# Optimization experiments

Hardware: AMD Instinct MI355X
Metric: run time of the kernel (lower is better)

The kernel has to match this reference:

```python
import jax, jax.numpy as jnp
import numpy as np

B, FEW, NN = 4096, 5, 64
D = 128            # embed_dim
NSYM = 100000
DM = 2 * D         # d_model = 256
DI = 2 * DM        # support-encoder inner = 512
H = 2 * DM         # LSTMCell hidden = 512
STEPS = 4          # process_steps


def setup_inputs() -> dict:
    key = jax.random.key(0)
    cnt = [0]
    def nk():
        cnt[0] += 1
        return jax.random.fold_in(key, cnt[0])
    def nrm(shape, scale=0.05):
        return jax.random.normal(nk(), shape, dtype=jnp.float32) * scale
    def ridx(shape):
        return jax.random.randint(nk(), shape, 0, NSYM, dtype=jnp.int32)
    inp = {}
    inp['q_l1'] = ridx((B, NN, 2)); inp['q_l2'] = ridx((B, NN, 2))
    inp['q_r1'] = ridx((B, NN, 2)); inp['q_r2'] = ridx((B, NN, 2))
    inp['s_l1'] = ridx((FEW, NN, 2)); inp['s_l2'] = ridx((FEW, NN, 2))
    inp['s_r1'] = ridx((FEW, NN, 2)); inp['s_r2'] = ridx((FEW, NN, 2))
    inp['q_deg_l'] = jax.random.randint(nk(), (B,), 1, NN, dtype=jnp.int32)
    inp['q_deg_r'] = jax.random.randint(nk(), (B,), 1, NN, dtype=jnp.int32)
    inp['s_deg_l'] = jax.random.randint(nk(), (FEW,), 1, NN, dtype=jnp.int32)
    inp['s_deg_r'] = jax.random.randint(nk(), (FEW,), 1, NN, dtype=jnp.int32)
    inp['emb'] = nrm((NSYM + 1, D)).at[NSYM].set(0.0)  # padding_idx row = 0
    inp['gcn_w'] = nrm((D, 2 * D))
    inp['gcn_wb'] = nrm((D,))
    inp['gcn_b'] = jnp.zeros((D,), jnp.float32)
    inp['hop_gate'] = jnp.ones((2,), jnp.float32)
    inp['attn_w'] = nrm((1, D))
    inp['attn_b'] = jnp.zeros((1,), jnp.float32)
    inp['p1_w'] = nrm((DI, DM)); inp['p1_b'] = jnp.zeros((DI,), jnp.float32)
    inp['p2_w'] = nrm((DM, DI)); inp['p2_b'] = jnp.zeros((DM,), jnp.float32)
    inp['ln_g'] = jnp.ones((DM,), jnp.float32); inp['ln_b'] = jnp.zeros((DM,), jnp.float32)
    inp['w_ih'] = nrm((4 * H, DM)); inp['w_hh'] = nrm((4 * H, H))
    inp['b_ih'] = jnp.zeros((4 * H,), jnp.float32); inp['b_hh'] = jnp.zeros((4 * H,), jnp.float32)
    return inp


def _neighbor_encoder(conn, emb, gcn_w, gcn_wb, gcn_b, attn_w, attn_b):
    # conn: [N, NN, 2] (relation id, entity id)
    e = emb[conn]                                     # [N, NN, 2, D]
    concat = e.reshape(conn.shape[0], conn.shape[1], 2 * D)  # cat(rel, ent)
    proj = concat @ gcn_w.T + gcn_wb + gcn_b          # [N, NN, D]
    scores = (proj @ attn_w.T + attn_b)[..., 0]       # [N, NN]
    w = jax.nn.softmax(scores, axis=1)[..., None]
    return jnp.tanh(jnp.sum(proj * w, axis=1))        # [N, D]


def _support_encoder(x, p1_w, p1_b, p2_w, p2_b, ln_g, ln_b):
    out = jax.nn.relu(x @ p1_w.T + p1_b) @ p2_w.T + p2_b
    z = out + x
    mu = jnp.mean(z, axis=-1, keepdims=True)
    var = jnp.var(z, axis=-1, keepdims=True)
    return (z - mu) / jnp.sqrt(var + 1e-6) * ln_g + ln_b


def _query_encoder(support_g, q, w_ih, w_hh, b_ih, b_hh):
    # matching-networks 'process' LSTM attention, STEPS fixed iterations
    h_r = jnp.zeros((q.shape[0], H), q.dtype)
    c = jnp.zeros_like(h_r)
    h = q
    for _ in range(STEPS):
        gates = q @ w_ih.T + b_ih + h_r @ w_hh.T + b_hh
        i, f, g, o = jnp.split(gates, 4, axis=-1)
        c = jax.nn.sigmoid(f) * c + jax.nn.sigmoid(i) * jnp.tanh(g)
        h_cell = jax.nn.sigmoid(o) * jnp.tanh(c)
        h = q + h_cell[:, :DM]
        attn = jax.nn.softmax(h @ support_g.T, axis=1)
        r = attn @ support_g
        h_r = jnp.concatenate([h, r], axis=1)
    return h


def reference(q_l1, q_l2, q_r1, q_r2, s_l1, s_l2, s_r1, s_r2,
              q_deg_l, q_deg_r, s_deg_l, s_deg_r,
              emb, gcn_w, gcn_wb, gcn_b, hop_gate, attn_w, attn_b,
              p1_w, p1_b, p2_w, p2_b, ln_g, ln_b, w_ih, w_hh, b_ih, b_hh):
    ne = lambda conn: _neighbor_encoder(conn, emb, gcn_w, gcn_wb, gcn_b, attn_w, attn_b)
    gw = jax.nn.softmax(hop_gate)
    q_left = gw[0] * ne(q_l1) + gw[1] * ne(q_l2)
    q_right = gw[0] * ne(q_r1) + gw[1] * ne(q_r2)
    s_left = gw[0] * ne(s_l1) + gw[1] * ne(s_l2)
    s_right = gw[0] * ne(s_r1) + gw[1] * ne(s_r2)
    query_neighbor = jnp.concatenate([q_left, q_right], axis=-1)    # [B, DM]
    support_neighbor = jnp.concatenate([s_left, s_right], axis=-1)  # [FEW, DM]
    support_g = _support_encoder(support_neighbor, p1_w, p1_b, p2_w, p2_b, ln_g, ln_b)
    query_g = _query_encoder(support_g, query_neighbor, w_ih, w_hh, b_ih, b_hh)
    support_m = jnp.mean(support_g, axis=0, keepdims=True)          # [1, DM]
    return (query_g @ support_m.T)[:, 0]                            # [B]
```

## Files before the change

kernel.cpp:

```cpp
#include <hip/hip_runtime.h>

typedef unsigned short bf16u;
typedef unsigned char u8;
typedef unsigned int u32;
typedef float f32x4 __attribute__((ext_vector_type(4)));
typedef short bf16x8 __attribute__((ext_vector_type(8)));

__device__ inline float sigmoidf_(float x) { return 1.f / (1.f + __expf(-x)); }
__device__ inline float tanhf_(float x) {
  float e = __expf(2.f * x);
  return 1.f - 2.f / (e + 1.f);
}
__device__ inline float b2f(bf16u u) { return __uint_as_float(((u32)u) << 16); }
__device__ inline bf16u f2b(float f) {
  u32 i = __float_as_uint(f);
  u32 r = (i + 0x7fffu + ((i >> 16) & 1u)) >> 16;
  return (bf16u)r;
}
__device__ inline u8 enc8(float v) {
  float q = fmaf(v, 512.f, 128.5f);
  q = fminf(fmaxf(q, 0.f), 255.f);
  return (u8)(int)q;
}
__device__ inline float ub0(u32 u) { return (float)(u & 0xffu); }
__device__ inline float ub1(u32 u) { return (float)((u >> 8) & 0xffu); }
__device__ inline float ub2(u32 u) { return (float)((u >> 16) & 0xffu); }
__device__ inline float ub3(u32 u) { return (float)(u >> 24); }

#define GLOAD16(gsrc, ldst)                                                   \
  __builtin_amdgcn_global_load_lds(                                           \
      (const __attribute__((address_space(1))) void*)(gsrc),                  \
      (__attribute__((address_space(3))) void*)(ldst), 16, 0, 0)

__global__ __launch_bounds__(256) void k_front(
    const float* __restrict__ emb, const float* __restrict__ gcn_w,
    const float* __restrict__ attn_w,
    const float* __restrict__ w_ih, const float* __restrict__ w_hh,
    const float* __restrict__ b_ih, const float* __restrict__ b_hh,
    u8* __restrict__ pr, u8* __restrict__ pe,
    float* __restrict__ srel, float* __restrict__ sent,
    bf16u* __restrict__ WWa, bf16u* __restrict__ WWb, float* __restrict__ bsum,
    bf16u* __restrict__ XX)
{
  const int blk = blockIdx.x, t = threadIdx.x;
  if (blk >= 1563) {
    const int b = blk - 1563;
    if (t < 59) {
      XX[(size_t)b * 576 + 517 + t] = 0;
      XX[(size_t)(b + 2048) * 576 + 517 + t] = 0;
    }
    float wi = w_ih[b * 256 + t];
    float wh = w_hh[b * 512 + t];
    WWa[(size_t)b * 576 + t] = f2b(wi);
    WWb[(size_t)b * 576 + t] = f2b(wi + wh);
    WWb[(size_t)b * 576 + 256 + t] = f2b(wh);
    if (t < 59) WWb[(size_t)b * 576 + 517 + t] = 0;
    if (t == 0) bsum[b] = b_ih[b] + b_hh[b];
    return;
  }
  const int row0 = blk << 6;
  __shared__ short As[64][136];
  __shared__ union PB {
    short B[128][136];
    u8 ob[64][272];
  } pb;
  __shared__ float us[256];
  #pragma unroll
  for (int s = 0; s < 8; ++s) {
    int f = s * 256 + t;
    int row = f >> 4, e0 = (f & 15) * 8;
    float4 v0 = *(const float4*)&gcn_w[row * 256 + e0];
    float4 v1 = *(const float4*)&gcn_w[row * 256 + e0 + 4];
    ushort4 p0, p1;
    p0.x = f2b(v0.x); p0.y = f2b(v0.y); p0.z = f2b(v0.z); p0.w = f2b(v0.w);
    p1.x = f2b(v1.x); p1.y = f2b(v1.y); p1.z = f2b(v1.z); p1.w = f2b(v1.w);
    *(ushort4*)&pb.B[row][e0] = p0;
    *(ushort4*)&pb.B[row][e0 + 4] = p1;
  }
  #pragma unroll
  for (int s = 0; s < 8; ++s) {
    int f = s * 256 + t;
    int row = f >> 5, q = f & 31;
    int gr = row0 + row; if (gr > 100000) gr = 100000;
    float4 v = *(const float4*)&emb[(size_t)gr * 128 + (q << 2)];
    ushort4 pk;
    pk.x = f2b(v.x); pk.y = f2b(v.y); pk.z = f2b(v.z); pk.w = f2b(v.w);
    *(ushort4*)&As[row][q << 2] = pk;
  }
  __syncthreads();
  if (t < 128) {
    float a = 0.f;
    #pragma unroll 8
    for (int d = 0; d < 128; ++d)
      a = fmaf(__uint_as_float(((u32)(unsigned short)pb.B[d][t]) << 16),
               attn_w[d], a);
    us[t] = a;
  }
  const int wave = t >> 6, lane = t & 63;
  const int quad = lane >> 4, l16 = lane & 15;
  const int wm = (wave >> 1) << 5, wn = (wave & 1) << 6;
  f32x4 acc0[2][4], acc1[2][4];
  #pragma unroll
  for (int i = 0; i < 2; ++i)
    #pragma unroll
    for (int j = 0; j < 4; ++j) {
      acc0[i][j] = (f32x4){0.f, 0.f, 0.f, 0.f};
      acc1[i][j] = (f32x4){0.f, 0.f, 0.f, 0.f};
    }
  #pragma unroll
  for (int kc = 0; kc < 4; ++kc) {
    bf16x8 af[2], bfr[4];
    #pragma unroll
    for (int i = 0; i < 2; ++i)
      af[i] = *(const bf16x8*)&As[wm + i * 16 + l16][kc * 32 + quad * 8];
    #pragma unroll
    for (int j = 0; j < 4; ++j)
      bfr[j] = *(const bf16x8*)&pb.B[wn + j * 16 + l16][kc * 32 + quad * 8];
    #pragma unroll
    for (int i = 0; i < 2; ++i)
      #pragma unroll
      for (int j = 0; j < 4; ++j)
        acc0[i][j] = __builtin_amdgcn_mfma_f32_16x16x32_bf16(af[i], bfr[j], acc0[i][j], 0, 0, 0);
  }
  __syncthreads();
  #pragma unroll
  for (int s = 0; s < 8; ++s) {
    int f = s * 256 + t;
    int row = f >> 4, e0 = (f & 15) * 8;
    float4 v0 = *(const float4*)&gcn_w[row * 256 + 128 + e0];
    float4 v1 = *(const float4*)&gcn_w[row * 256 + 128 + e0 + 4];
    ushort4 p0, p1;
    p0.x = f2b(v0.x); p0.y = f2b(v0.y); p0.z = f2b(v0.z); p0.w = f2b(v0.w);
    p1.x = f2b(v1.x); p1.y = f2b(v1.y); p1.z = f2b(v1.z); p1.w = f2b(v1.w);
    *(ushort4*)&pb.B[row][e0] = p0;
    *(ushort4*)&pb.B[row][e0 + 4] = p1;
  }
  __syncthreads();
  if (t < 128) {
    float a = 0.f;
    #pragma unroll 8
    for (int d = 0; d < 128; ++d)
      a = fmaf(__uint_as_float(((u32)(unsigned short)pb.B[d][t]) << 16),
               attn_w[d], a);
    us[128 + t] = a;
  }
  #pragma unroll
  for (int kc = 0; kc < 4; ++kc) {
    bf16x8 af[2], bfr[4];
    #pragma unroll
    for (int i = 0; i < 2; ++i)
      af[i] = *(const bf16x8*)&As[wm + i * 16 + l16][kc * 32 + quad * 8];
    #pragma unroll
    for (int j = 0; j < 4; ++j)
      bfr[j] = *(const bf16x8*)&pb.B[wn + j * 16 + l16][kc * 32 + quad * 8];
    #pragma unroll
    for (int i = 0; i < 2; ++i)
      #pragma unroll
      for (int j = 0; j < 4; ++j)
        acc1[i][j] = __builtin_amdgcn_mfma_f32_16x16x32_bf16(af[i], bfr[j], acc1[i][j], 0, 0, 0);
  }
  __syncthreads();
  {
    const int row = t >> 2, l = t & 3;
    int gr = row0 + row; if (gr > 100000) gr = 100000;
    const short* ar = &As[row][l * 32];
    const float* u0 = &us[l * 32];
    const float* u1 = &us[128 + l * 32];
    float p0 = 0.f, p1 = 0.f;
    #pragma unroll
    for (int i = 0; i < 32; ++i) {
      float e = __uint_as_float(((u32)(unsigned short)ar[i]) << 16);
      p0 += e * u0[i];
      p1 += e * u1[i];
    }
    p0 += __shfl_xor(p0, 1, 64); p0 += __shfl_xor(p0, 2, 64);
    p1 += __shfl_xor(p1, 1, 64); p1 += __shfl_xor(p1, 2, 64);
    if (l == 0) { srel[gr] = p0; sent[gr] = p1; }
  }
  #pragma unroll
  for (int j = 0; j < 4; ++j) {
    const int col = wn + j * 16 + l16;
    #pragma unroll
    for (int i = 0; i < 2; ++i) {
      #pragma unroll
      for (int r = 0; r < 4; ++r) {
        int row = wm + i * 16 + quad * 4 + r;
        pb.ob[row][col] = enc8(acc0[i][j][r]);
        pb.ob[row][128 + col] = enc8(acc1[i][j][r]);
      }
    }
  }
  __syncthreads();
  #pragma unroll
  for (int s = 0; s < 4; ++s) {
    int c = s * 256 + t;
    int row = c >> 4, part = c & 15;
    int gr = row0 + row;
    if (gr <= 100000) {
      uint4 v = *(const uint4*)&pb.ob[row][part * 16];
      if (part < 8) *(uint4*)&pr[(size_t)gr * 128 + part * 16] = v;
      else          *(uint4*)&pe[(size_t)gr * 128 + (part - 8) * 16] = v;
    }
  }
}

__global__ __launch_bounds__(256) void k_neighbor(
    const int* __restrict__ q_l1, const int* __restrict__ q_l2,
    const int* __restrict__ q_r1, const int* __restrict__ q_r2,
    const int* __restrict__ s_l1, const int* __restrict__ s_l2,
    const int* __restrict__ s_r1, const int* __restrict__ s_r2,
    const u8* __restrict__ pr, const u8* __restrict__ pe,
    const float* __restrict__ srel, const float* __restrict__ sent,
    const float* __restrict__ gcn_wb, const float* __restrict__ gcn_b,
    const float* __restrict__ hop_gate,
    float* __restrict__ qn, float* __restrict__ sn, bf16u* __restrict__ XX)
{
  const int b = blockIdx.x, t = threadIdx.x;
  const int *cA, *cB; float* outp; bf16u* xxp; int n, coloff;
  if (b < 4096)      { cA = q_l1; cB = q_l2; n = b;        outp = qn; xxp = XX; coloff = 0; }
  else if (b < 8192) { cA = q_r1; cB = q_r2; n = b - 4096; outp = qn; xxp = XX; coloff = 128; }
  else if (b < 8197) { cA = s_l1; cB = s_l2; n = b - 8192; outp = sn; xxp = 0;  coloff = 0; }
  else               { cA = s_r1; cB = s_r2; n = b - 8197; outp = sn; xxp = 0;  coloff = 128; }

  __shared__ float wS[2][64];
  __shared__ float red[256][17];

  const int hop = t >> 7, g = (t >> 3) & 15, p = t & 7;
  const int* connG = hop ? cB : cA;

  int2 pairs[4];
  #pragma unroll
  for (int kk = 0; kk < 4; ++kk)
    pairs[kk] = *(const int2*)&connG[(n * 64 + g + (kk << 4)) * 2];

  float vR = 0.f, vE = 0.f;
  if (t < 128) {
    const int sh = t >> 6, nn = t & 63;
    const int* connS = sh ? cB : cA;
    int2 sp = *(const int2*)&connS[(n * 64 + nn) * 2];
    vR = srel[sp.x];
    vE = sent[sp.y];
  }

  uint4 ra[4], rb[4];
  #pragma unroll
  for (int kk = 0; kk < 4; ++kk) {
    ra[kk] = *(const uint4*)&pr[(size_t)pairs[kk].x * 128 + p * 16];
    rb[kk] = *(const uint4*)&pe[(size_t)pairs[kk].y * 128 + p * 16];
  }

  if (t < 128) {
    const int sh = t >> 6, nn = t & 63;
    float sc = vR + vE;
    float m = sc;
    #pragma unroll
    for (int off = 32; off; off >>= 1) m = fmaxf(m, __shfl_xor(m, off, 64));
    float e = __expf(sc - m);
    float s = e;
    #pragma unroll
    for (int off = 32; off; off >>= 1) s += __shfl_xor(s, off, 64);
    wS[sh][nn] = e / s;
  }
  __syncthreads();

  float a[16];
  #pragma unroll
  for (int c = 0; c < 16; ++c) a[c] = 0.f;
  #pragma unroll
  for (int kk = 0; kk < 4; ++kk) {
    const float wk = wS[hop][g + (kk << 4)];
    const uint4 A = ra[kk], Bv = rb[kk];
    a[0]  += wk * (ub0(A.x) + ub0(Bv.x));
    a[1]  += wk * (ub1(A.x) + ub1(Bv.x));
    a[2]  += wk * (ub2(A.x) + ub2(Bv.x));
    a[3]  += wk * (ub3(A.x) + ub3(Bv.x));
    a[4]  += wk * (ub0(A.y) + ub0(Bv.y));
    a[5]  += wk * (ub1(A.y) + ub1(Bv.y));
    a[6]  += wk * (ub2(A.y) + ub2(Bv.y));
    a[7]  += wk * (ub3(A.y) + ub3(Bv.y));
    a[8]  += wk * (ub0(A.z) + ub0(Bv.z));
    a[9]  += wk * (ub1(A.z) + ub1(Bv.z));
    a[10] += wk * (ub2(A.z) + ub2(Bv.z));
    a[11] += wk * (ub3(A.z) + ub3(Bv.z));
    a[12] += wk * (ub0(A.w) + ub0(Bv.w));
    a[13] += wk * (ub1(A.w) + ub1(Bv.w));
    a[14] += wk * (ub2(A.w) + ub2(Bv.w));
    a[15] += wk * (ub3(A.w) + ub3(Bv.w));
  }
  #pragma unroll
  for (int c = 0; c < 16; ++c) red[t][c] = a[c];
  __syncthreads();

  if (t < 128) {
    const int d = t, pp = d >> 4, cc = d & 15;
    float sA = 0.f, sB = 0.f;
    #pragma unroll
    for (int gg = 0; gg < 16; ++gg) {
      sA += red[gg * 8 + pp][cc];
      sB += red[128 + gg * 8 + pp][cc];
    }
    float accA = sA * (1.f / 512.f) - 0.5f;
    float accB = sB * (1.f / 512.f) - 0.5f;
    float bias = gcn_wb[d] + gcn_b[d];
    float g0 = hop_gate[0], g1 = hop_gate[1];
    float mx = fmaxf(g0, g1);
    float e0 = __expf(g0 - mx), e1 = __expf(g1 - mx);
    float inv = 1.f / (e0 + e1);
    float v = e0 * inv * tanhf_(bias + accA) + e1 * inv * tanhf_(bias + accB);
    outp[n * 256 + coloff + d] = v;
    if (xxp) xxp[(size_t)n * 576 + coloff + d] = f2b(v);
  }
}

__global__ __launch_bounds__(256) void k_sup1(
    const float* __restrict__ sn, const float* __restrict__ p1_w,
    const float* __restrict__ p1_b, float* __restrict__ h1)
{
  const int r = blockIdx.x >> 3, j0 = (blockIdx.x & 7) << 6;
  const int t = threadIdx.x;
  __shared__ float xs[256];
  xs[t] = sn[r * 256 + t];
  __syncthreads();
  const int j = j0 + (t >> 2), q = t & 3;
  const float* wr = p1_w + (size_t)j * 256 + q * 64;
  float acc = 0.f;
  #pragma unroll
  for (int k = 0; k < 64; ++k) acc += xs[q * 64 + k] * wr[k];
  acc += __shfl_xor(acc, 1, 64);
  acc += __shfl_xor(acc, 2, 64);
  if (q == 0) h1[r * 512 + j] = fmaxf(acc + p1_b[j], 0.f);
}

__global__ __launch_bounds__(256) void k_sup2(
    const float* __restrict__ sn, const float* __restrict__ h1,
    const float* __restrict__ p2_w, const float* __restrict__ p2_b,
    const float* __restrict__ ln_g, const float* __restrict__ ln_b,
    float* __restrict__ sg)
{
  const int r = blockIdx.x, t = threadIdx.x;
  const int lane = t & 63, wave = t >> 6;
  __shared__ float hs[512];
  __shared__ float zs[256];
  __shared__ float r1[4], r2[4];
  hs[t] = h1[r * 512 + t];
  hs[t + 256] = h1[r * 512 + 256 + t];
  __syncthreads();
  const int q = t & 3;
  #pragma unroll
  for (int jc = 0; jc < 4; ++jc) {
    int j = jc * 64 + (t >> 2);
    const float* wr = p2_w + (size_t)j * 512 + q * 128;
    float acc = 0.f;
    #pragma unroll
    for (int k = 0; k < 128; ++k) acc += hs[q * 128 + k] * wr[k];
    acc += __shfl_xor(acc, 1, 64);
    acc += __shfl_xor(acc, 2, 64);
    if (q == 0) zs[j] = acc + p2_b[j] + sn[r * 256 + j];
  }
  __syncthreads();
  float v = zs[t];
  float s1 = v, s2 = v * v;
  #pragma unroll
  for (int off = 32; off; off >>= 1) { s1 += __shfl_xor(s1, off, 64); s2 += __shfl_xor(s2, off, 64); }
  if (lane == 0) { r1[wave] = s1; r2[wave] = s2; }
  __syncthreads();
  float S1 = r1[0] + r1[1] + r1[2] + r1[3];
  float S2 = r2[0] + r2[1] + r2[2] + r2[3];
  float mu = S1 * (1.f / 256.f);
  float var = S2 * (1.f / 256.f) - mu * mu;
  sg[r * 256 + t] = (v - mu) * rsqrtf(var + 1e-6f) * ln_g[t] + ln_b[t];
}

__global__ __launch_bounds__(256) void k_gates_mfma(
    const bf16u* __restrict__ XX, const bf16u* __restrict__ WW,
    const float* __restrict__ bsum, bf16u* __restrict__ gates, int kchunks,
    const float* __restrict__ sg, const float* __restrict__ w_hh,
    bf16u* __restrict__ WWbo, float* __restrict__ sm, int dosg2)
{
  const int t = threadIdx.x;
  const int wave = t >> 6, lane = t & 63;
  const int quad = lane >> 4, l16 = lane & 15;
  const int wm = (wave >> 1) << 6, wn = (wave & 1) << 6;
  const int lin = (blockIdx.x & 7) * 56 + (blockIdx.x >> 3);
  const int row0 = (lin / 14) << 7;
  const int col0 = (lin % 14) << 7;
  __shared__ short As[2][128][64];
  __shared__ short Bs[2][128][64];

  if (dosg2 && blockIdx.x < 32) {
    float (*s5)[256] = (float(*)[256])&As[0][0][0];
    const int blk = blockIdx.x;
    for (int i = t; i < 1280; i += 256) s5[i >> 8][i & 255] = sg[i];
    __syncthreads();
    if (blk == 0)
      sm[t] = (s5[0][t] + s5[1][t] + s5[2][t] + s5[3][t] + s5[4][t]) * 0.2f;
    const int j = (blk << 6) + (t >> 2), q = t & 3;
    const float4* wr = (const float4*)(w_hh + (size_t)j * 512 + 256 + q * 64);
    float a[5] = {0.f, 0.f, 0.f, 0.f, 0.f};
    #pragma unroll
    for (int kk = 0; kk < 16; ++kk) {
      float4 w = wr[kk];
      int k = q * 64 + kk * 4;
      #pragma unroll
      for (int r = 0; r < 5; ++r)
        a[r] += s5[r][k] * w.x + s5[r][k+1] * w.y + s5[r][k+2] * w.z + s5[r][k+3] * w.w;
    }
    #pragma unroll
    for (int r = 0; r < 5; ++r) {
      a[r] += __shfl_xor(a[r], 1, 64);
      a[r] += __shfl_xor(a[r], 2, 64);
    }
    if (q == 0) {
      #pragma unroll
      for (int r = 0; r < 5; ++r)
        WWbo[(size_t)j * 576 + 512 + r] = f2b(a[r]);
    }
    __syncthreads();
  }

  f32x4 acc[4][4];
  #pragma unroll
  for (int i = 0; i < 4; ++i)
    #pragma unroll
    for (int j = 0; j < 4; ++j) acc[i][j] = (f32x4){0.f, 0.f, 0.f, 0.f};

  int offX[4], offW[4];
  #pragma unroll
  for (int e = 0; e < 4; ++e) {
    int row = wave * 32 + e * 8 + (lane >> 3);
    int sw = (lane & 7) ^ (lane >> 3);
    offX[e] = (row0 + row) * 576 + sw * 8;
    offW[e] = (col0 + row) * 576 + sw * 8;
  }
  char* aBase = (char*)&As[0][0][0] + wave * 4096;
  char* bBase = (char*)&Bs[0][0][0] + wave * 4096;

  #define STAGE(buf, kc)                                                      \
    {                                                                         \
      const int kof_ = (kc) * 64;                                             \
      _Pragma("unroll")                                                       \
      for (int e = 0; e < 4; ++e) {                                           \
        GLOAD16(XX + offX[e] + kof_, aBase + (buf) * 16384 + e * 1024);       \
        GLOAD16(WW + offW[e] + kof_, bBase + (buf) * 16384 + e * 1024);       \
      }                                                                       \
    }

  STAGE(0, 0);
  __syncthreads();

  for (int kc = 0; kc < kchunks; ++kc) {
    const int cur = kc & 1;
    if (kc + 1 < kchunks) STAGE(cur ^ 1, kc + 1);
    #pragma unroll
    for (int kc2 = 0; kc2 < 2; ++kc2) {
      bf16x8 af[4], bfr[4];
      #pragma unroll
      for (int i = 0; i < 4; ++i)
        af[i] = *(const bf16x8*)&As[cur][wm + i * 16 + l16]
                                       [(((kc2 << 2) + quad) ^ (l16 & 7)) << 3];
      #pragma unroll
      for (int j = 0; j < 4; ++j)
        bfr[j] = *(const bf16x8*)&Bs[cur][wn + j * 16 + l16]
                                        [(((kc2 << 2) + quad) ^ (l16 & 7)) << 3];
      #pragma unroll
      for (int i = 0; i < 4; ++i)
        #pragma unroll
        for (int j = 0; j < 4; ++j)
          acc[i][j] = __builtin_amdgcn_mfma_f32_16x16x32_bf16(af[i], bfr[j], acc[i][j], 0, 0, 0);
    }
    __syncthreads();
  }
  #undef STAGE

  #pragma unroll
  for (int j = 0; j < 4; ++j) {
    const int col = col0 + wn + j * 16 + l16;
    const float bs = bsum[col];
    #pragma unroll
    for (int i = 0; i < 4; ++i) {
      #pragma unroll
      for (int r = 0; r < 4; ++r) {
        int row = row0 + wm + i * 16 + quad * 4 + r;
        gates[(size_t)row * 2048 + col] = f2b(acc[i][j][r] + bs);
      }
    }
  }
}

__global__ __launch_bounds__(256) void k_cell(
    const bf16u* __restrict__ gates, const float* __restrict__ qn,
    float* __restrict__ c, bf16u* __restrict__ XX,
    const float* __restrict__ sg, const float* __restrict__ sm,
    float* __restrict__ out, int step)
{
  __shared__ float red[4][6];
  const int b = blockIdx.x, t = threadIdx.x;
  const int lane = t & 63, wave = t >> 6;
  const bf16u* g = gates + (size_t)b * 2048;
  float i0 = b2f(g[t]),       f0 = b2f(g[512 + t]), gg0 = b2f(g[1024 + t]), o0 = b2f(g[1536 + t]);
  float i1 = b2f(g[256 + t]), f1 = b2f(g[768 + t]), gg1 = b2f(g[1280 + t]);
  float co0 = step ? c[b * 512 + t] : 0.f;
  float co1 = step ? c[b * 512 + 256 + t] : 0.f;
  float c0 = sigmoidf_(f0) * co0 + sigmoidf_(i0) * tanhf_(gg0);
  float c1 = sigmoidf_(f1) * co1 + sigmoidf_(i1) * tanhf_(gg1);
  if (step < 3) {
    c[b * 512 + t] = c0;
    c[b * 512 + 256 + t] = c1;
  }
  float hcv = sigmoidf_(o0) * tanhf_(c0);
  float h = qn[b * 256 + t] + hcv;
  if (step < 3) {
    XX[(size_t)b * 576 + 256 + t] = f2b(hcv);
    float dots[5];
    #pragma unroll
    for (int s = 0; s < 5; ++s) dots[s] = h * sg[s * 256 + t];
    #pragma unroll
    for (int off = 32; off; off >>= 1) {
      #pragma unroll
      for (int s = 0; s < 5; ++s) dots[s] += __shfl_xor(dots[s], off, 64);
    }
    if (lane == 0) {
      #pragma unroll
      for (int s = 0; s < 5; ++s) red[wave][s] = dots[s];
    }
    __syncthreads();
    #pragma unroll
    for (int s = 0; s < 5; ++s)
      dots[s] = red[0][s] + red[1][s] + red[2][s] + red[3][s];
    float m = dots[0];
    #pragma unroll
    for (int s = 1; s < 5; ++s) m = fmaxf(m, dots[s]);
    float sum = 0.f;
    #pragma unroll
    for (int s = 0; s < 5; ++s) sum += __expf(dots[s] - m);
    if (t < 5) {
      float dv = (t == 1) ? dots[1] : (t == 2) ? dots[2] : (t == 3) ? dots[3]
               : (t == 4) ? dots[4] : dots[0];
      XX[(size_t)b * 576 + 512 + t] = f2b(__expf(dv - m) / sum);
    }
  } else {
    float v = h * sm[t];
    #pragma unroll
    for (int off = 32; off; off >>= 1) v += __shfl_xor(v, off, 64);
    if (lane == 0) red[wave][0] = v;
    __syncthreads();
    if (t == 0) out[b] = red[0][0] + red[1][0] + red[2][0] + red[3][0];
  }
}

extern "C" void kernel_launch(void* const* d_in, const int* in_sizes, int n_in,
                              void* d_out, int out_size, void* d_ws, size_t ws_size,
                              hipStream_t stream)
{
  (void)in_sizes; (void)n_in; (void)out_size; (void)ws_size;
  const int *q_l1 = (const int*)d_in[0], *q_l2 = (const int*)d_in[1];
  const int *q_r1 = (const int*)d_in[2], *q_r2 = (const int*)d_in[3];
  const int *s_l1 = (const int*)d_in[4], *s_l2 = (const int*)d_in[5];
  const int *s_r1 = (const int*)d_in[6], *s_r2 = (const int*)d_in[7];
  const float* emb      = (const float*)d_in[12];
  const float* gcn_w    = (const float*)d_in[13];
  const float* gcn_wb   = (const float*)d_in[14];
  const float* gcn_b    = (const float*)d_in[15];
  const float* hop_gate = (const float*)d_in[16];
  const float* attn_w   = (const float*)d_in[17];
  const float* p1_w = (const float*)d_in[19];
  const float* p1_b = (const float*)d_in[20];
  const float* p2_w = (const float*)d_in[21];
  const float* p2_b = (const float*)d_in[22];
  const float* ln_g = (const float*)d_in[23];
  const float* ln_b = (const float*)d_in[24];
  const float* w_ih = (const float*)d_in[25];
  const float* w_hh = (const float*)d_in[26];
  const float* b_ih = (const float*)d_in[27];
  const float* b_hh = (const float*)d_in[28];

  char* base = (char*)d_ws;
  size_t off = 0;
  auto alloc = [&](size_t bytes) -> char* {
    char* r = base + off;
    off = (off + bytes + 255) & ~(size_t)255;
    return r;
  };
  u8* pr       = (u8*)alloc(100001ull * 128);
  u8* pe       = (u8*)alloc(100001ull * 128);
  float* srel  = (float*)alloc(100001ull * 4);
  float* sent  = (float*)alloc(100001ull * 4);
  float* qn    = (float*)alloc(4096ull * 256 * 4);
  float* sn    = (float*)alloc(5 * 256 * 4);
  float* sg    = (float*)alloc(5 * 256 * 4);
  float* sm    = (float*)alloc(256 * 4);
  float* h1b   = (float*)alloc(5 * 512 * 4);
  bf16u* XX    = (bf16u*)alloc(4096ull * 576 * 2);
  bf16u* WWa   = (bf16u*)alloc(2048ull * 576 * 2);
  bf16u* WWb   = (bf16u*)alloc(2048ull * 576 * 2);
  float* bsum  = (float*)alloc(2048 * 4);
  bf16u* gates = (bf16u*)alloc(4096ull * 2048 * 2);
  float* cbuf  = (float*)alloc(4096ull * 512 * 4);

  k_front<<<3611, 256, 0, stream>>>(emb, gcn_w, attn_w, w_ih, w_hh, b_ih, b_hh,
                                    pr, pe, srel, sent, WWa, WWb, bsum, XX);
  k_neighbor<<<8202, 256, 0, stream>>>(q_l1, q_l2, q_r1, q_r2, s_l1, s_l2, s_r1, s_r2,
                                       pr, pe, srel, sent, gcn_wb, gcn_b, hop_gate,
                                       qn, sn, XX);
  k_sup1<<<40, 256, 0, stream>>>(sn, p1_w, p1_b, h1b);
  k_sup2<<<5, 256, 0, stream>>>(sn, h1b, p2_w, p2_b, ln_g, ln_b, sg);

  for (int step = 0; step < 4; ++step) {
    if (step == 0)
      k_gates_mfma<<<448, 256, 0, stream>>>(XX, WWa, bsum, gates, 4,
                                            sg, w_hh, WWb, sm, 1);
    else
      k_gates_mfma<<<448, 256, 0, stream>>>(XX, WWb, bsum, gates, 9,
                                            sg, w_hh, WWb, sm, 0);
    k_cell<<<4096, 256, 0, stream>>>(gates, qn, cbuf, XX, sg, sm, (float*)d_out, step);
  }
}
```

Measured before the change: 332.8 us.

## Pre-convert gcn_w to swizzled bf16 once and DMA it into LDS

Adds a small prep kernel that converts gcn_w to bf16 a single time, in an XOR-swizzled layout. k_front then loads the weight tiles directly into LDS with global_load_lds, instead of having each of ~1563 blocks redo the fp32-to-bf16 conversion. The per-block attn_w·W dot products are replaced by reducing the MFMA accumulators against attn_w with shuffles, and the padded LDS rows become swizzled unpadded rows to avoid bank conflicts. This saves redundant conversion and scalar loops, at the cost of one extra launch and a different rounding order for the attention scores.

New measurement: 324.6 us, median of 2. 1.03x faster.

```diff
diff --git a/kernel.cpp b/kernel.cpp
--- a/kernel.cpp
+++ b/kernel.cpp
@@ -32,8 +32,25 @@
       (const __attribute__((address_space(1))) void*)(gsrc),                  \
       (__attribute__((address_space(3))) void*)(ldst), 16, 0, 0)
 
+__global__ __launch_bounds__(256) void k_vprep(
+    const float* __restrict__ gcn_w, bf16u* __restrict__ Vp)
+{
+  const int g = blockIdx.x * 256 + threadIdx.x;
+  const int half = g >> 11, rem = g & 2047;
+  const int r = rem >> 4, qs = rem & 15;
+  const int ls = qs ^ (r & 15);
+  const float* src = gcn_w + r * 256 + half * 128 + ls * 8;
+  float4 v0 = *(const float4*)src;
+  float4 v1 = *(const float4*)(src + 4);
+  ushort4 p0, p1;
+  p0.x = f2b(v0.x); p0.y = f2b(v0.y); p0.z = f2b(v0.z); p0.w = f2b(v0.w);
+  p1.x = f2b(v1.x); p1.y = f2b(v1.y); p1.z = f2b(v1.z); p1.w = f2b(v1.w);
+  *(ushort4*)(Vp + (size_t)g * 8) = p0;
+  *(ushort4*)(Vp + (size_t)g * 8 + 4) = p1;
+}
+
 __global__ __launch_bounds__(256) void k_front(
-    const float* __restrict__ emb, const float* __restrict__ gcn_w,
+    const float* __restrict__ emb, const bf16u* __restrict__ Vp,
     const float* __restrict__ attn_w,
     const float* __restrict__ w_ih, const float* __restrict__ w_hh,
     const float* __restrict__ b_ih, const float* __restrict__ b_hh,
@@ -61,21 +78,22 @@
   const int row0 = blk << 6;
   __shared__ short As[64][136];
   __shared__ union PB {
-    short B[128][136];
+    short B[128][128];
     u8 ob[64][272];
   } pb;
-  __shared__ float us[256];
-  #pragma unroll
-  for (int s = 0; s < 8; ++s) {
-    int f = s * 256 + t;
-    int row = f >> 4, e0 = (f & 15) * 8;
-    float4 v0 = *(const float4*)&gcn_w[row * 256 + e0];
-    float4 v1 = *(const float4*)&gcn_w[row * 256 + e0 + 4];
-    ushort4 p0, p1;
-    p0.x = f2b(v0.x); p0.y = f2b(v0.y); p0.z = f2b(v0.z); p0.w = f2b(v0.w);
-    p1.x = f2b(v1.x); p1.y = f2b(v1.y); p1.z = f2b(v1.z); p1.w = f2b(v1.w);
-    *(ushort4*)&pb.B[row][e0] = p0;
-    *(ushort4*)&pb.B[row][e0 + 4] = p1;
+  __shared__ float scp[2][2][64];
+
+  const int wave = t >> 6, lane = t & 63;
+  const int quad = lane >> 4, l16 = lane & 15;
+  const int wm = (wave >> 1) << 5, wn = (wave & 1) << 6;
+
+  {
+    char* lbase = (char*)&pb.B[0][0] + wave * 8192;
+    #pragma unroll
+    for (int e = 0; e < 8; ++e) {
+      int s = wave * 512 + e * 64 + lane;
+      GLOAD16(Vp + (size_t)s * 8, lbase + e * 1024);
+    }
   }
   #pragma unroll
   for (int s = 0; s < 8; ++s) {
@@ -87,18 +105,10 @@
     pk.x = f2b(v.x); pk.y = f2b(v.y); pk.z = f2b(v.z); pk.w = f2b(v.w);
     *(ushort4*)&As[row][q << 2] = pk;
   }
-  __syncthreads();
-  if (t < 128) {
-    float a = 0.f;
-    #pragma unroll 8
-    for (int d = 0; d < 128; ++d)
-      a = fmaf(__uint_as_float(((u32)(unsigned short)pb.B[d][t]) << 16),
-               attn_w[d], a);
-    us[t] = a;
-  }
-  const int wave = t >> 6, lane = t & 63;
-  const int quad = lane >> 4, l16 = lane & 15;
-  const int wm = (wave >> 1) << 5, wn = (wave & 1) << 6;
+  float aw[4];
+  #pragma unroll
+  for (int j = 0; j < 4; ++j) aw[j] = attn_w[wn + j * 16 + l16];
+
   f32x4 acc0[2][4], acc1[2][4];
   #pragma unroll
   for (int i = 0; i < 2; ++i)
@@ -107,6 +117,7 @@
       acc0[i][j] = (f32x4){0.f, 0.f, 0.f, 0.f};
       acc1[i][j] = (f32x4){0.f, 0.f, 0.f, 0.f};
     }
+  __syncthreads();
   #pragma unroll
   for (int kc = 0; kc < 4; ++kc) {
     bf16x8 af[2], bfr[4];
@@ -115,7 +126,8 @@
       af[i] = *(const bf16x8*)&As[wm + i * 16 + l16][kc * 32 + quad * 8];
     #pragma unroll
     for (int j = 0; j < 4; ++j)
-      bfr[j] = *(const bf16x8*)&pb.B[wn + j * 16 + l16][kc * 32 + quad * 8];
+      bfr[j] = *(const bf16x8*)&pb.B[wn + j * 16 + l16]
+                                    [((kc * 4 + quad) ^ l16) * 8];
     #pragma unroll
     for (int i = 0; i < 2; ++i)
       #pragma unroll
@@ -123,27 +135,15 @@
         acc0[i][j] = __builtin_amdgcn_mfma_f32_16x16x32_bf16(af[i], bfr[j], acc0[i][j], 0, 0, 0);
   }
   __syncthreads();
-  #pragma unroll
-  for (int s = 0; s < 8; ++s) {
-    int f = s * 256 + t;
-    int row = f >> 4, e0 = (f & 15) * 8;
-    float4 v0 = *(const float4*)&gcn_w[row * 256 + 128 + e0];
-    float4 v1 = *(const float4*)&gcn_w[row * 256 + 128 + e0 + 4];
-    ushort4 p0, p1;
-    p0.x = f2b(v0.x); p0.y = f2b(v0.y); p0.z = f2b(v0.z); p0.w = f2b(v0.w);
-    p1.x = f2b(v1.x); p1.y = f2b(v1.y); p1.z = f2b(v1.z); p1.w = f2b(v1.w);
-    *(ushort4*)&pb.B[row][e0] = p0;
-    *(ushort4*)&pb.B[row][e0 + 4] = p1;
-  }
-  __syncthreads();
-  if (t < 128) {
-    float a = 0.f;
-    #pragma unroll 8
-    for (int d = 0; d < 128; ++d)
-      a = fmaf(__uint_as_float(((u32)(unsigned short)pb.B[d][t]) << 16),
-               attn_w[d], a);
-    us[128 + t] = a;
-  }
+  {
+    char* lbase = (char*)&pb.B[0][0] + wave * 8192;
+    #pragma unroll
+    for (int e = 0; e < 8; ++e) {
+      int s = wave * 512 + e * 64 + lane;
+      GLOAD16(Vp + 16384 + (size_t)s * 8, lbase + e * 1024);
+    }
+  }
+  __syncthreads();
   #pragma unroll
   for (int kc = 0; kc < 4; ++kc) {
     bf16x8 af[2], bfr[4];
@@ -152,31 +152,37 @@
       af[i] = *(const bf16x8*)&As[wm + i * 16 + l16][kc * 32 + quad * 8];
     #pragma unroll
     for (int j = 0; j < 4; ++j)
-      bfr[j] = *(const bf16x8*)&pb.B[wn + j * 16 + l16][kc * 32 + quad * 8];
+      bfr[j] = *(const bf16x8*)&pb.B[wn + j * 16 + l16]
+                                    [((kc * 4 + quad) ^ l16) * 8];
     #pragma unroll
     for (int i = 0; i < 2; ++i)
       #pragma unroll
       for (int j = 0; j < 4; ++j)
         acc1[i][j] = __builtin_amdgcn_mfma_f32_16x16x32_bf16(af[i], bfr[j], acc1[i][j], 0, 0, 0);
   }
-  __syncthreads();
   {
-    const int row = t >> 2, l = t & 3;
-    int gr = row0 + row; if (gr > 100000) gr = 100000;
-    const short* ar = &As[row][l * 32];
-    const float* u0 = &us[l * 32];
-    const float* u1 = &us[128 + l * 32];
-    float p0 = 0.f, p1 = 0.f;
-    #pragma unroll
-    for (int i = 0; i < 32; ++i) {
-      float e = __uint_as_float(((u32)(unsigned short)ar[i]) << 16);
-      p0 += e * u0[i];
-      p1 += e * u1[i];
-    }
-    p0 += __shfl_xor(p0, 1, 64); p0 += __shfl_xor(p0, 2, 64);
-    p1 += __shfl_xor(p1, 1, 64); p1 += __shfl_xor(p1, 2, 64);
-    if (l == 0) { srel[gr] = p0; sent[gr] = p1; }
-  }
+    #pragma unroll
+    for (int i = 0; i < 2; ++i) {
+      #pragma unroll
+      for (int r = 0; r < 4; ++r) {
+        float t0 = acc0[i][0][r] * aw[0] + acc0[i][1][r] * aw[1] +
+                   acc0[i][2][r] * aw[2] + acc0[i][3][r] * aw[3];
+        float t1 = acc1[i][0][r] * aw[0] + acc1[i][1][r] * aw[1] +
+                   acc1[i][2][r] * aw[2] + acc1[i][3][r] * aw[3];
+        #pragma unroll
+        for (int m = 1; m < 16; m <<= 1) {
+          t0 += __shfl_xor(t0, m, 64);
+          t1 += __shfl_xor(t1, m, 64);
+        }
+        if (l16 == 0) {
+          int row = wm + i * 16 + quad * 4 + r;
+          scp[0][wn >> 6][row] = t0;
+          scp[1][wn >> 6][row] = t1;
+        }
+      }
+    }
+  }
+  __syncthreads();
   #pragma unroll
   for (int j = 0; j < 4; ++j) {
     const int col = wn + j * 16 + l16;
@@ -188,6 +194,13 @@
         pb.ob[row][col] = enc8(acc0[i][j][r]);
         pb.ob[row][128 + col] = enc8(acc1[i][j][r]);
       }
+    }
+  }
+  if (t < 64) {
+    int gr = row0 + t;
+    if (gr <= 100000) {
+      srel[gr] = scp[0][0][t] + scp[0][1][t];
+      sent[gr] = scp[1][0][t] + scp[1][1][t];
     }
   }
   __syncthreads();
@@ -585,6 +598,7 @@
   u8* pe       = (u8*)alloc(100001ull * 128);
   float* srel  = (float*)alloc(100001ull * 4);
   float* sent  = (float*)alloc(100001ull * 4);
+  bf16u* Vp    = (bf16u*)alloc(2ull * 16384 * 2);
   float* qn    = (float*)alloc(4096ull * 256 * 4);
   float* sn    = (float*)alloc(5 * 256 * 4);
   float* sg    = (float*)alloc(5 * 256 * 4);
@@ -597,7 +611,8 @@
   bf16u* gates = (bf16u*)alloc(4096ull * 2048 * 2);
   float* cbuf  = (float*)alloc(4096ull * 512 * 4);
 
-  k_front<<<3611, 256, 0, stream>>>(emb, gcn_w, attn_w, w_ih, w_hh, b_ih, b_hh,
+  k_vprep<<<16, 256, 0, stream>>>(gcn_w, Vp);
+  k_front<<<3611, 256, 0, stream>>>(emb, Vp, attn_w, w_ih, w_hh, b_ih, b_hh,
                                     pr, pe, srel, sent, WWa, WWb, bsum, XX);
   k_neighbor<<<8202, 256, 0, stream>>>(q_l1, q_l2, q_r1, q_r2, s_l1, s_l2, s_r1, s_r2,
                                        pr, pe, srel, sent, gcn_wb, gcn_b, hop_gate,
```
